# Kernel optimization log

Measured on AMD Instinct MI355X. Metric: run time of the kernel, lower is better.

## Reference

```python
import jax, jax.numpy as jnp
import numpy as np

# Module config (from init_kwargs)
OUTPUT_TYPE = "all"   # 'class', 'box', or 'all'
CONF = 0.25
RATIO = 1.0
END2END = False


def setup_inputs() -> dict:
    key = jax.random.key(0)
    k1, k2 = jax.random.split(key)
    N, C = 2_000_000, 80
    post_result = jax.random.uniform(k1, (N, C), dtype=jnp.float32)
    pre_post_boxes = jax.random.uniform(k2, (N, 4), dtype=jnp.float32)
    return {"post_result": post_result, "pre_post_boxes": pre_post_boxes}


def reference(post_result, pre_post_boxes):
    # Number of candidates considered (static: ratio is a Python constant)
    M = int(post_result.shape[0] * RATIO)
    pr = post_result[:M]
    boxes = pre_post_boxes[:M]  # [M, 4]

    # Per-candidate confidence score
    scores = pr[:, 0] if END2END else jnp.max(pr, axis=1)  # [M]

    # The original loop breaks at the FIRST score < conf. That is a cumulative
    # AND of (score >= conf): keep[i] = all(scores[:i+1] >= conf).
    keep = jnp.cumprod((scores >= CONF).astype(pr.dtype))  # [M]

    total = jnp.zeros((), dtype=pr.dtype)
    if OUTPUT_TYPE in ("class", "all"):
        total = total + jnp.sum(keep * scores)
    if OUTPUT_TYPE in ("box", "all"):
        total = total + jnp.sum(keep * jnp.sum(boxes, axis=1))
    return total
```

## Files before the change

kernel.cpp:

```cpp
#include <hip/hip_runtime.h>
#include <hip/hip_bf16.h>

#define NCLS 80
#define CONF_T 0.25f
#define P1_BLOCKS 2048
#define P1_THREADS 256
#define TILE_ROWS 128
#define TILE_F4 ((TILE_ROWS * NCLS) / 4)
#define F4_PER_THREAD (TILE_F4 / P1_THREADS)

typedef __attribute__((address_space(1))) const void gvoid_t;
typedef __attribute__((address_space(3))) void lvoid_t;


__global__ void init_fail(int* fail, int N) { *fail = N; }

__device__ __forceinline__ float row_val_global(const float* __restrict__ pr,
                                                const float* __restrict__ boxes,
                                                int row, float* score_out) {
    const float4* p = (const float4*)(pr + (size_t)row * NCLS);
    float m = -INFINITY;
#pragma unroll
    for (int k = 0; k < NCLS / 4; ++k) {
        float4 v = p[k];
        m = fmaxf(m, fmaxf(fmaxf(v.x, v.y), fmaxf(v.z, v.w)));
    }
    float4 b = ((const float4*)boxes)[row];
    *score_out = m;
    return m + b.x + b.y + b.z + b.w;
}

__device__ __forceinline__ float block_reduce_sum(float v) {
#pragma unroll
    for (int off = 32; off > 0; off >>= 1) v += __shfl_down(v, off, 64);
    __shared__ float sred[P1_THREADS / 64];
    int lane = threadIdx.x & 63;
    int wid  = threadIdx.x >> 6;
    if (lane == 0) sred[wid] = v;
    __syncthreads();
    float total = 0.f;
    if (threadIdx.x == 0) {
#pragma unroll
        for (int w = 0; w < P1_THREADS / 64; ++w) total += sred[w];
    }
    return total;
}

__global__ __launch_bounds__(P1_THREADS) void pass1(const float* __restrict__ pr,
                                                    const float* __restrict__ boxes,
                                                    float* __restrict__ partials,
                                                    int* __restrict__ fail,
                                                    int N, int tiles_per_block) {
    __shared__ float4 sbuf[TILE_F4];

    const int t = (int)threadIdx.x;
    const int tile0 = blockIdx.x * tiles_per_block;
    float acc = 0.f;

    for (int ti = 0; ti < tiles_per_block; ++ti) {
        const int row0 = (tile0 + ti) * TILE_ROWS;
        if (row0 >= N) break;

        if (row0 + TILE_ROWS <= N) {
            const float4* gp = (const float4*)pr + (size_t)row0 * (NCLS / 4);
#pragma unroll
            for (int k = 0; k < F4_PER_THREAD; ++k) {
                int i4 = t + k * P1_THREADS;
                __builtin_amdgcn_global_load_lds((gvoid_t*)(gp + i4),
                                                 (lvoid_t*)(sbuf + i4), 16, 0, 0);
            }
            __syncthreads();

            const int r = t >> 1, h = t & 1;
            const float4* rowp = (const float4*)((const float*)sbuf + r * NCLS + h * (NCLS / 2));
            float m = -INFINITY;
#pragma unroll
            for (int j = 0; j < NCLS / 8; ++j) {
                float4 v = rowp[j];
                m = fmaxf(m, fmaxf(fmaxf(v.x, v.y), fmaxf(v.z, v.w)));
            }
            m = fmaxf(m, __shfl_xor(m, 1, 64));
            if (h == 0) {
                int row = row0 + r;
                float4 b = ((const float4*)boxes)[row];
                if (m < CONF_T) atomicMin(fail, row);
                acc += m + b.x + b.y + b.z + b.w;
            }
            __syncthreads();
        } else {
            int ce = min(row0 + TILE_ROWS, N);
            for (int row = row0 + t; row < ce; row += P1_THREADS) {
                float score;
                float v = row_val_global(pr, boxes, row, &score);
                if (score < CONF_T) atomicMin(fail, row);
                acc += v;
            }
        }
    }

    float tot = block_reduce_sum(acc);
    if (t == 0) partials[blockIdx.x] = tot;
}

__global__ __launch_bounds__(P1_THREADS) void pass2(const float* __restrict__ pr,
                                                    const float* __restrict__ boxes,
                                                    const float* __restrict__ partials,
                                                    const int* __restrict__ fail,
                                                    float* __restrict__ out,
                                                    int N, int R) {
    int ff = *fail;
    if (ff > N) ff = N;
    if (ff < 0) ff = 0;

    int full, start;
    if (ff >= N) { full = P1_BLOCKS; start = N; }
    else         { full = ff / R;    start = full * R; }

    float acc = 0.f;
    for (int c = (int)threadIdx.x; c < full; c += P1_THREADS) acc += partials[c];
    for (int row = start + (int)threadIdx.x; row < ff; row += P1_THREADS) {
        float score;
        acc += row_val_global(pr, boxes, row, &score);
    }
    float tot = block_reduce_sum(acc);
    if (threadIdx.x == 0) *out = tot;
}

extern "C" void kernel_launch(void* const* d_in, const int* in_sizes, int n_in,
                              void* d_out, int out_size, void* d_ws, size_t ws_size,
                              hipStream_t stream) {
    const float* pr    = (const float*)d_in[0];
    const float* boxes = (const float*)d_in[1];
    float* out = (float*)d_out;

    int N = in_sizes[1] / 4;
    int tiles_total = (N + TILE_ROWS - 1) / TILE_ROWS;
    int tiles_per_block = (tiles_total + P1_BLOCKS - 1) / P1_BLOCKS;
    int R = tiles_per_block * TILE_ROWS;

    int*   fail     = (int*)d_ws;
    float* partials = (float*)((char*)d_ws + 256);

    init_fail<<<1, 1, 0, stream>>>(fail, N);
    pass1<<<P1_BLOCKS, P1_THREADS, 0, stream>>>(pr, boxes, partials, fail, N, tiles_per_block);
    pass2<<<1, P1_THREADS, 0, stream>>>(pr, boxes, partials, fail, out, N, R);
}
```

Measured before the change: 817.9 us.

## Replace LDS-staged tiles with direct per-row global loads by 4-lane groups

The pass1 kernel no longer stages 128-row tiles into shared memory with global_load_lds and two barriers per tile. Each group of 4 lanes now reads one row straight from global memory as five float4 loads with interleaved offsets, reduces the max with two xor shuffles, and each lane adds one box component. The aim is to drop LDS traffic and __syncthreads stalls and keep more loads in flight, at the cost of less regular coalescing per wavefront. Rows per block are rounded to a multiple of 64, which changes the partition that pass2 relies on.

```diff
diff --git a/kernel.cpp b/kernel.cpp
--- a/kernel.cpp
+++ b/kernel.cpp
@@ -1,16 +1,9 @@
 #include <hip/hip_runtime.h>
-#include <hip/hip_bf16.h>
 
 #define NCLS 80
 #define CONF_T 0.25f
 #define P1_BLOCKS 2048
 #define P1_THREADS 256
-#define TILE_ROWS 128
-#define TILE_F4 ((TILE_ROWS * NCLS) / 4)
-#define F4_PER_THREAD (TILE_F4 / P1_THREADS)
-
-typedef __attribute__((address_space(1))) const void gvoid_t;
-typedef __attribute__((address_space(3))) void lvoid_t;
 
 
 __global__ void init_fail(int* fail, int N) { *fail = N; }
@@ -50,50 +43,41 @@
                                                     const float* __restrict__ boxes,
                                                     float* __restrict__ partials,
                                                     int* __restrict__ fail,
-                                                    int N, int tiles_per_block) {
-    __shared__ float4 sbuf[TILE_F4];
+                                                    int N, int R) {
+    const int t    = (int)threadIdx.x;
+    const int lane = t & 63;
+    const int w    = t >> 6;
+    const int sub  = lane & 3;
+    const int g    = lane >> 2;
 
-    const int t = (int)threadIdx.x;
-    const int tile0 = blockIdx.x * tiles_per_block;
+    const int row0   = (int)blockIdx.x * R;
+    const int rowEnd = min(row0 + R, N);
+
     float acc = 0.f;
 
-    for (int ti = 0; ti < tiles_per_block; ++ti) {
-        const int row0 = (tile0 + ti) * TILE_ROWS;
-        if (row0 >= N) break;
+    for (int base = row0 + (w << 4); base < rowEnd; base += 64) {
+        const int row = base + g;
+        if (row < rowEnd) {
+            const float4* p = (const float4*)(pr + (size_t)row * NCLS) + sub;
+            float4 v0 = p[0];
+            float4 v1 = p[4];
+            float4 v2 = p[8];
+            float4 v3 = p[12];
+            float4 v4 = p[16];
+            float m0 = fmaxf(fmaxf(v0.x, v0.y), fmaxf(v0.z, v0.w));
+            float m1 = fmaxf(fmaxf(v1.x, v1.y), fmaxf(v1.z, v1.w));
+            float m2 = fmaxf(fmaxf(v2.x, v2.y), fmaxf(v2.z, v2.w));
+            float m3 = fmaxf(fmaxf(v3.x, v3.y), fmaxf(v3.z, v3.w));
+            float m4 = fmaxf(fmaxf(v4.x, v4.y), fmaxf(v4.z, v4.w));
+            float m  = fmaxf(fmaxf(fmaxf(m0, m1), fmaxf(m2, m3)), m4);
+            m = fmaxf(m, __shfl_xor(m, 1, 64));
+            m = fmaxf(m, __shfl_xor(m, 2, 64));
 
-        if (row0 + TILE_ROWS <= N) {
-            const float4* gp = (const float4*)pr + (size_t)row0 * (NCLS / 4);
-#pragma unroll
-            for (int k = 0; k < F4_PER_THREAD; ++k) {
-                int i4 = t + k * P1_THREADS;
-                __builtin_amdgcn_global_load_lds((gvoid_t*)(gp + i4),
-                                                 (lvoid_t*)(sbuf + i4), 16, 0, 0);
-            }
-            __syncthreads();
+            acc += boxes[(size_t)row * 4 + sub];
 
-            const int r = t >> 1, h = t & 1;
-            const float4* rowp = (const float4*)((const float*)sbuf + r * NCLS + h * (NCLS / 2));
-            float m = -INFINITY;
-#pragma unroll
-            for (int j = 0; j < NCLS / 8; ++j) {
-                float4 v = rowp[j];
-                m = fmaxf(m, fmaxf(fmaxf(v.x, v.y), fmaxf(v.z, v.w)));
-            }
-            m = fmaxf(m, __shfl_xor(m, 1, 64));
-            if (h == 0) {
-                int row = row0 + r;
-                float4 b = ((const float4*)boxes)[row];
+            if (sub == 0) {
                 if (m < CONF_T) atomicMin(fail, row);
-                acc += m + b.x + b.y + b.z + b.w;
-            }
-            __syncthreads();
-        } else {
-            int ce = min(row0 + TILE_ROWS, N);
-            for (int row = row0 + t; row < ce; row += P1_THREADS) {
-                float score;
-                float v = row_val_global(pr, boxes, row, &score);
-                if (score < CONF_T) atomicMin(fail, row);
-                acc += v;
+                acc += m;
             }
         }
     }
@@ -134,14 +118,14 @@
     float* out = (float*)d_out;
 
     int N = in_sizes[1] / 4;
-    int tiles_total = (N + TILE_ROWS - 1) / TILE_ROWS;
-    int tiles_per_block = (tiles_total + P1_BLOCKS - 1) / P1_BLOCKS;
-    int R = tiles_per_block * TILE_ROWS;
+
+    int rpb = (N + P1_BLOCKS - 1) / P1_BLOCKS;
+    int R   = (rpb + 63) & ~63;
 
     int*   fail     = (int*)d_ws;
     float* partials = (float*)((char*)d_ws + 256);
 
     init_fail<<<1, 1, 0, stream>>>(fail, N);
-    pass1<<<P1_BLOCKS, P1_THREADS, 0, stream>>>(pr, boxes, partials, fail, N, tiles_per_block);
+    pass1<<<P1_BLOCKS, P1_THREADS, 0, stream>>>(pr, boxes, partials, fail, N, R);
     pass2<<<1, P1_THREADS, 0, stream>>>(pr, boxes, partials, fail, out, N, R);
 }
```

Result: no change. 818.2 us (+0.0%).
